# Optimization experiments

Measured on AMD Instinct MI355X. Metric: run time of the kernel, lower is better.

Reference implementation:

```python
import jax, jax.numpy as jnp
import numpy as np

ALPHA = 0.5        # self._alpha
MAX_COEFF = 10.0   # self._max_coeff
SHARPNESS = 5      # self._loss_sharpness

N_VARS = 1_000_000
N_CLAUSES = 4_000_000
N_EDGES = 12_000_000


def setup_inputs() -> dict:
    key = jax.random.key(0)
    k1, k2, k3, k4 = jax.random.split(key, 4)
    variable_prediction = jax.random.uniform(k1, (N_VARS, 1), dtype=jnp.float32)
    lits = jax.random.randint(k2, (N_EDGES,), 0, N_VARS, dtype=jnp.int32)
    clauses = jax.random.randint(k3, (N_EDGES,), 0, N_CLAUSES, dtype=jnp.int32)
    graph_map = jnp.stack([lits, clauses])  # [2, E]
    # literal polarity: +1 (positive literal) or -1 (negated literal)
    edge_feature = jnp.where(jax.random.bernoulli(k4, 0.5, (N_EDGES, 1)), 1.0, -1.0).astype(jnp.float32)
    return {
        "variable_prediction": variable_prediction,
        "graph_map": graph_map,
        "edge_feature": edge_feature,
        "num_clauses": N_CLAUSES,
        "global_step": jnp.array([100.0], dtype=jnp.float32),
        "eps": jnp.array([1e-10], dtype=jnp.float32),
    }


def reference(variable_prediction, graph_map, edge_feature, num_clauses, global_step, eps):
    # temperature coefficient: min(step^alpha, max_coeff)
    coeff = jnp.minimum(global_step ** ALPHA, MAX_COEFF)  # [1]
    lits = graph_map[0]     # [E] variable index per edge
    clauses = graph_map[1]  # [E] clause index per edge
    ef = edge_feature[:, 0]  # [E]

    # sparse mm (signed variable mask @ prediction) == signed gather
    edge_values = ef * variable_prediction[lits, 0]          # [E]
    edge_values = edge_values + (1.0 - ef) * 0.5             # negated literal -> 1 - p
    weights = jnp.exp(coeff * edge_values)                   # [E]

    # sparse mm (function mask @ .) == scatter-add over clauses
    nominator = jax.ops.segment_sum(weights * edge_values, clauses, num_segments=num_clauses)
    denominator = jax.ops.segment_sum(weights, clauses, num_segments=num_clauses)

    clause_value = denominator / jnp.maximum(nominator, eps)
    clause_value = 1.0 + (clause_value - 1.0) ** SHARPNESS
    return jnp.mean(jnp.log(jnp.maximum(clause_value, eps)))
```

## Files before the change

kernel.cpp:

```cpp
#include <hip/hip_runtime.h>
#include <math.h>


constexpr int   N_CLAUSES_C = 4000000;
constexpr int   BKT_SHIFT   = 12;
constexpr int   BKT_CLS     = 1 << BKT_SHIFT;
constexpr int   NB_TOTAL    = (N_CLAUSES_C + BKT_CLS - 1) >> BKT_SHIFT;
constexpr int   CAP         = 13056;
constexpr int   SC_THREADS  = 1024;
constexpr int   BATCH       = 8192;
constexpr int   NBATCH      = 3;
constexpr int   SC_CHUNK    = BATCH * NBATCH;
constexpr int   PR_THREADS  = 512;

typedef int v4i __attribute__((ext_vector_type(4)));

__device__ __forceinline__ uint32_t ev_enc(float ev) {
    return (__float_as_uint(ev) + 0x400u) >> 11;
}
__device__ __forceinline__ float ev_dec(uint32_t q) {
    return __uint_as_float(q << 11);
}

__device__ __forceinline__ void load_pair(const int* __restrict__ cls,
                                          const int* __restrict__ lits,
                                          int base, int c1, int (&cc)[8], int (&ll)[8]) {
    if (base + 8 <= c1) {
        v4i ca = __builtin_nontemporal_load((const v4i*)(cls  + base));
        v4i cb = __builtin_nontemporal_load((const v4i*)(cls  + base + 4));
        v4i la = __builtin_nontemporal_load((const v4i*)(lits + base));
        v4i lb = __builtin_nontemporal_load((const v4i*)(lits + base + 4));
        #pragma unroll
        for (int i = 0; i < 4; ++i) {
            cc[i] = ca[i]; cc[4 + i] = cb[i];
            ll[i] = la[i]; ll[4 + i] = lb[i];
        }
    } else {
        #pragma unroll
        for (int i = 0; i < 8; ++i) {
            int e = base + i;
            if (e < c1) { cc[i] = cls[e]; ll[i] = lits[e]; }
            else        { cc[i] = -1;     ll[i] = 0;       }
        }
    }
}

__device__ __forceinline__ void load_ef(const int* __restrict__ efi,
                                        int base, int c1, int (&ss)[8]) {
    if (base + 8 <= c1) {
        v4i fa = __builtin_nontemporal_load((const v4i*)(efi + base));
        v4i fb = __builtin_nontemporal_load((const v4i*)(efi + base + 4));
        #pragma unroll
        for (int i = 0; i < 4; ++i) { ss[i] = fa[i]; ss[4 + i] = fb[i]; }
    } else {
        #pragma unroll
        for (int i = 0; i < 8; ++i) { int e = base + i; ss[i] = (e < c1) ? efi[e] : 0; }
    }
}

__global__ __launch_bounds__(SC_THREADS, 8) void
scatter_kernel(const float* __restrict__ vp,
               const int* __restrict__ lits,
               const int* __restrict__ cls,
               const int* __restrict__ efi,
               uint32_t* __restrict__ payload,
               uint32_t* __restrict__ cursors,
               int n_edges, int b_lo, int b_hi) {
    __shared__ uint32_t bh[1024];
    __shared__ uint32_t bOff[1024];
    __shared__ uint32_t bb[NB_TOTAL];
    __shared__ uint32_t buf[BATCH];
    __shared__ uint16_t bufB[BATCH];
    __shared__ uint32_t totalS;

    const int tid  = threadIdx.x;
    const int lane = tid & 63;
    const int wv   = tid >> 6;
    const int nbp  = b_hi - b_lo;
    const int c0   = blockIdx.x * SC_CHUNK;
    const int c1   = min(n_edges, c0 + SC_CHUNK);
    const int nb   = (c1 - c0 + BATCH - 1) / BATCH;

    int cc[8], ll[8];
    load_pair(cls, lits, c0 + tid * 8, c1, cc, ll);
    bh[tid] = 0;
    __syncthreads();

    for (int k = 0; k < nb; ++k) {
        const int base = c0 + k * BATCH + tid * 8;

        int ss[8];
        load_ef(efi, base, c1, ss);
        float vv[8];
        #pragma unroll
        for (int i = 0; i < 8; ++i) vv[i] = (cc[i] >= 0) ? vp[ll[i]] : 0.0f;

        uint32_t meta[8];
        #pragma unroll
        for (int i = 0; i < 8; ++i) {
            meta[i] = 0xFFC00000u;
            if (cc[i] >= 0) {
                int b = cc[i] >> BKT_SHIFT;
                if (b >= b_lo && b < b_hi) {
                    uint32_t ib = (uint32_t)(b - b_lo);
                    uint32_t r  = atomicAdd(&bh[ib], 1u);
                    if (r < 1024u)
                        meta[i] = ((uint32_t)cc[i] & 4095u) | (r << 12) | (ib << 22);
                }
            }
        }
        __syncthreads();

        if (wv == 0) {
            const int jb = lane * 16;
            uint32_t t = 0;
            #pragma unroll
            for (int i = 0; i < 16; ++i) t += bh[jb + i];
            uint32_t x = t;
            #pragma unroll
            for (int d = 1; d < 64; d <<= 1) {
                uint32_t n = __shfl_up(x, (unsigned)d, 64);
                if (lane >= d) x += n;
            }
            uint32_t run = x - t;
            #pragma unroll
            for (int i = 0; i < 16; ++i) {
                uint32_t v = bh[jb + i];
                bOff[jb + i] = run;
                run += v;
            }
            if (lane == 63) totalS = x;
        } else {
            for (int i = tid - 64; i < nbp; i += SC_THREADS - 64) {
                uint32_t v = bh[i];
                bb[i] = v ? atomicAdd(&cursors[b_lo + i], v) : 0u;
            }
        }
        __syncthreads();

        #pragma unroll
        for (int i = 0; i < 8; ++i) {
            uint32_t ib = meta[i] >> 22;
            if (ib < 1023u) {
                float ev = (ss[i] >= 0) ? vv[i] : (1.0f - vv[i]);
                uint32_t s = bOff[ib] + ((meta[i] >> 12) & 1023u);
                buf[s]  = (ev_enc(ev) << BKT_SHIFT) | (meta[i] & 4095u);
                bufB[s] = (uint16_t)ib;
            }
        }
        bh[tid] = 0;
        if (k + 1 < nb)
            load_pair(cls, lits, c0 + (k + 1) * BATCH + tid * 8, c1, cc, ll);
        __syncthreads();

        const uint32_t tS = totalS;
        for (uint32_t s = tid; s < tS; s += SC_THREADS) {
            uint32_t ib   = bufB[s];
            uint32_t gpos = bb[ib] + (s - bOff[ib]);
            if (gpos < (uint32_t)CAP)
                payload[(size_t)ib * CAP + gpos] = buf[s];
        }
        __syncthreads();
    }
}

__global__ __launch_bounds__(PR_THREADS) void
process_kernel(const uint32_t* __restrict__ payload,
               const uint32_t* __restrict__ cursors,
               const float* __restrict__ gstep,
               const float* __restrict__ epsp,
               double* __restrict__ acc,
               int b_lo) {
    __shared__ uint32_t offp[BKT_CLS / 2];
    __shared__ uint32_t srt[CAP];
    __shared__ uint32_t wscan[8];
    __shared__ double   wsum[8];
    const int tid  = threadIdx.x;
    const int lane = tid & 63;
    const int wv   = tid >> 6;
    const int b    = b_lo + blockIdx.x;

    for (int j = tid; j < BKT_CLS / 2; j += PR_THREADS) offp[j] = 0;
    __syncthreads();

    const uint32_t cnt = min(cursors[b], (uint32_t)CAP);
    const uint32_t* pl = payload + (size_t)blockIdx.x * CAP;
    const uint32_t nv = cnt >> 2;

    for (uint32_t k = tid; k < nv; k += PR_THREADS) {
        uint4 p4 = ((const uint4*)pl)[k];
        uint32_t c;
        c = p4.x & (BKT_CLS - 1); atomicAdd(&offp[c >> 1], 1u << ((c & 1) << 4));
        c = p4.y & (BKT_CLS - 1); atomicAdd(&offp[c >> 1], 1u << ((c & 1) << 4));
        c = p4.z & (BKT_CLS - 1); atomicAdd(&offp[c >> 1], 1u << ((c & 1) << 4));
        c = p4.w & (BKT_CLS - 1); atomicAdd(&offp[c >> 1], 1u << ((c & 1) << 4));
    }
    for (uint32_t k = (nv << 2) + tid; k < cnt; k += PR_THREADS) {
        uint32_t c = pl[k] & (BKT_CLS - 1);
        atomicAdd(&offp[c >> 1], 1u << ((c & 1) << 4));
    }
    __syncthreads();

    uint32_t pk[4];
    const int jb = tid * 4;
    uint32_t t = 0;
    #pragma unroll
    for (int i = 0; i < 4; ++i) {
        pk[i] = offp[jb + i];
        t += (pk[i] & 0xFFFFu) + (pk[i] >> 16);
    }
    uint32_t x = t;
    #pragma unroll
    for (int d = 1; d < 64; d <<= 1) {
        uint32_t n = __shfl_up(x, (unsigned)d, 64);
        if (lane >= d) x += n;
    }
    if (lane == 63) wscan[wv] = x;
    __syncthreads();
    if (tid == 0) {
        uint32_t r = 0;
        #pragma unroll
        for (int w = 0; w < 8; ++w) { uint32_t tm = wscan[w]; wscan[w] = r; r += tm; }
    }
    __syncthreads();
    uint32_t run = (x - t) + wscan[wv];
    #pragma unroll
    for (int i = 0; i < 4; ++i) {
        uint32_t lo = pk[i] & 0xFFFFu, hi = pk[i] >> 16;
        offp[jb + i] = run | ((run + lo) << 16);
        run += lo + hi;
    }
    __syncthreads();

    for (uint32_t k = tid; k < nv; k += PR_THREADS) {
        uint4 p4 = ((const uint4*)pl)[k];
        #pragma unroll
        for (int j = 0; j < 4; ++j) {
            uint32_t p = (j == 0) ? p4.x : (j == 1) ? p4.y : (j == 2) ? p4.z : p4.w;
            uint32_t c = p & (BKT_CLS - 1);
            uint32_t sh = (c & 1) << 4;
            uint32_t r = atomicAdd(&offp[c >> 1], 1u << sh);
            srt[(r >> sh) & 0xFFFFu] = p;
        }
    }
    for (uint32_t k = (nv << 2) + tid; k < cnt; k += PR_THREADS) {
        uint32_t p = pl[k];
        uint32_t c = p & (BKT_CLS - 1);
        uint32_t sh = (c & 1) << 4;
        uint32_t r = atomicAdd(&offp[c >> 1], 1u << sh);
        srt[(r >> sh) & 0xFFFFu] = p;
    }
    __syncthreads();

    const float coeff = fminf(sqrtf(gstep[0]), 10.0f);
    const float eps   = epsp[0];
    const int gbase = b << BKT_SHIFT;
    double local = 0.0;
    for (int j = tid; j < BKT_CLS; j += PR_THREADS) {
        if (gbase + j < N_CLAUSES_C) {
            uint32_t e = (offp[j >> 1] >> ((j & 1) << 4)) & 0xFFFFu;
            uint32_t s = 0;
            if (j > 0) {
                int jm = j - 1;
                s = (offp[jm >> 1] >> ((jm & 1) << 4)) & 0xFFFFu;
            }
            float nom = 0.f, den = 0.f;
            for (uint32_t k = s; k < e; ++k) {
                float ev = ev_dec(srt[k] >> BKT_SHIFT);
                float w  = __expf(coeff * ev);
                nom = fmaf(w, ev, nom);
                den += w;
            }
            float cv = den / fmaxf(nom, eps);
            float tt = cv - 1.0f;
            float t2 = tt * tt;
            float cv2 = 1.0f + t2 * t2 * tt;
            local += (double)__logf(fmaxf(cv2, eps));
        }
    }
    #pragma unroll
    for (int off = 32; off > 0; off >>= 1) local += __shfl_down(local, off, 64);
    if (lane == 0) wsum[wv] = local;
    __syncthreads();
    if (tid == 0) {
        double s = 0.0;
        #pragma unroll
        for (int w = 0; w < 8; ++w) s += wsum[w];
        unsafeAtomicAdd(acc, s);
    }
}

__global__ void finalize_kernel(const double* __restrict__ acc,
                                const int* __restrict__ ncp,
                                float* __restrict__ out) {
    if (threadIdx.x == 0 && blockIdx.x == 0)
        out[0] = (float)(acc[0] / (double)ncp[0]);
}

extern "C" void kernel_launch(void* const* d_in, const int* in_sizes, int n_in,
                              void* d_out, int out_size, void* d_ws, size_t ws_size,
                              hipStream_t stream) {
    const float* vp    = (const float*)d_in[0];
    const int*   gmap  = (const int*)d_in[1];
    const float* ef    = (const float*)d_in[2];
    const int*   ncp   = (const int*)d_in[3];
    const float* gstep = (const float*)d_in[4];
    const float* epsp  = (const float*)d_in[5];
    float*       out   = (float*)d_out;

    const int n_edges = in_sizes[1] / 2;
    const int* lits = gmap;
    const int* cls  = gmap + n_edges;

    int P = 8;
    int nbp_max = (NB_TOTAL + 7) / 8;
    size_t cursors_off_w = (size_t)nbp_max * CAP;
    size_t acc_off_w = (cursors_off_w + NB_TOTAL + 1) & ~(size_t)1;
    const int cands[4] = {1, 2, 4, 8};
    for (int ci = 0; ci < 4; ++ci) {
        int cand = cands[ci];
        int nm = (NB_TOTAL + cand - 1) / cand;
        size_t pw = (size_t)nm * CAP;
        size_t cw = pw + NB_TOTAL;
        size_t aw = (cw + 1) & ~(size_t)1;
        size_t need = aw * 4 + 8;
        if (need <= ws_size) { P = cand; nbp_max = nm; cursors_off_w = pw; acc_off_w = aw; break; }
    }

    uint32_t* payload = (uint32_t*)d_ws;
    uint32_t* cursors = payload + cursors_off_w;
    double*   acc     = (double*)((uint32_t*)d_ws + acc_off_w);

    hipMemsetAsync(cursors, 0, (acc_off_w - cursors_off_w) * 4 + 8, stream);

    const int sc_blocks = (n_edges + SC_CHUNK - 1) / SC_CHUNK;
    for (int p = 0; p < P; ++p) {
        int b_lo = p * nbp_max;
        int b_hi = min(NB_TOTAL, b_lo + nbp_max);
        if (b_lo >= b_hi) continue;
        scatter_kernel<<<sc_blocks, SC_THREADS, 0, stream>>>(
            vp, lits, cls, (const int*)ef, payload, cursors, n_edges, b_lo, b_hi);
        process_kernel<<<b_hi - b_lo, PR_THREADS, 0, stream>>>(
            payload, cursors, gstep, epsp, acc, b_lo);
    }
    finalize_kernel<<<1, 64, 0, stream>>>(acc, ncp, out);
}
```

Before: 175.2 us.

## Double clause bucket width and split bucket processing across two half-blocks

Scatter buckets now cover 8192 clauses each instead of 4096, which halves the bucket count and the per-block histogram, offset and global cursor atomic work in the scatter kernel. The edge-value encoding gives up one more mantissa bit to make room for the wider clause index. The process kernel launches two blocks per bucket; each reads the whole bucket payload but only sorts and reduces the half of the clauses it owns, which keeps shared memory per block near its previous size. The cost is that every payload word is read twice, plus slightly coarser quantisation and new overflow clamps on the sort buffer.

```diff
diff --git a/kernel.cpp b/kernel.cpp
--- a/kernel.cpp
+++ b/kernel.cpp
@@ -3,10 +3,12 @@
 
 
 constexpr int   N_CLAUSES_C = 4000000;
-constexpr int   BKT_SHIFT   = 12;
+constexpr int   BKT_SHIFT   = 13;
 constexpr int   BKT_CLS     = 1 << BKT_SHIFT;
 constexpr int   NB_TOTAL    = (N_CLAUSES_C + BKT_CLS - 1) >> BKT_SHIFT;
-constexpr int   CAP         = 13056;
+constexpr int   CAP         = 25728;
+constexpr int   SUB_CLS     = 4096;
+constexpr int   SRT_CAP     = 13824;
 constexpr int   SC_THREADS  = 1024;
 constexpr int   BATCH       = 8192;
 constexpr int   NBATCH      = 3;
@@ -16,10 +18,10 @@
 typedef int v4i __attribute__((ext_vector_type(4)));
 
 __device__ __forceinline__ uint32_t ev_enc(float ev) {
-    return (__float_as_uint(ev) + 0x400u) >> 11;
+    return (__float_as_uint(ev) + 0x800u) >> 12;
 }
 __device__ __forceinline__ float ev_dec(uint32_t q) {
-    return __uint_as_float(q << 11);
+    return __uint_as_float(q << 12);
 }
 
 __device__ __forceinline__ void load_pair(const int* __restrict__ cls,
@@ -66,9 +68,9 @@
                uint32_t* __restrict__ payload,
                uint32_t* __restrict__ cursors,
                int n_edges, int b_lo, int b_hi) {
-    __shared__ uint32_t bh[1024];
-    __shared__ uint32_t bOff[1024];
-    __shared__ uint32_t bb[NB_TOTAL];
+    __shared__ uint32_t bh[512];
+    __shared__ uint32_t bOff[512];
+    __shared__ uint32_t bb[512];
     __shared__ uint32_t buf[BATCH];
     __shared__ uint16_t bufB[BATCH];
     __shared__ uint32_t totalS;
@@ -83,7 +85,7 @@
 
     int cc[8], ll[8];
     load_pair(cls, lits, c0 + tid * 8, c1, cc, ll);
-    bh[tid] = 0;
+    if (tid < 512) bh[tid] = 0;
     __syncthreads();
 
     for (int k = 0; k < nb; ++k) {
@@ -98,24 +100,24 @@
         uint32_t meta[8];
         #pragma unroll
         for (int i = 0; i < 8; ++i) {
-            meta[i] = 0xFFC00000u;
+            meta[i] = 0xFF800000u;
             if (cc[i] >= 0) {
                 int b = cc[i] >> BKT_SHIFT;
                 if (b >= b_lo && b < b_hi) {
                     uint32_t ib = (uint32_t)(b - b_lo);
                     uint32_t r  = atomicAdd(&bh[ib], 1u);
                     if (r < 1024u)
-                        meta[i] = ((uint32_t)cc[i] & 4095u) | (r << 12) | (ib << 22);
+                        meta[i] = ((uint32_t)cc[i] & 8191u) | (r << 13) | (ib << 23);
                 }
             }
         }
         __syncthreads();
 
         if (wv == 0) {
-            const int jb = lane * 16;
+            const int jb = lane * 8;
             uint32_t t = 0;
             #pragma unroll
-            for (int i = 0; i < 16; ++i) t += bh[jb + i];
+            for (int i = 0; i < 8; ++i) t += bh[jb + i];
             uint32_t x = t;
             #pragma unroll
             for (int d = 1; d < 64; d <<= 1) {
@@ -124,7 +126,7 @@
             }
             uint32_t run = x - t;
             #pragma unroll
-            for (int i = 0; i < 16; ++i) {
+            for (int i = 0; i < 8; ++i) {
                 uint32_t v = bh[jb + i];
                 bOff[jb + i] = run;
                 run += v;
@@ -140,15 +142,15 @@
 
         #pragma unroll
         for (int i = 0; i < 8; ++i) {
-            uint32_t ib = meta[i] >> 22;
-            if (ib < 1023u) {
+            uint32_t ib = meta[i] >> 23;
+            if (ib < 511u) {
                 float ev = (ss[i] >= 0) ? vv[i] : (1.0f - vv[i]);
-                uint32_t s = bOff[ib] + ((meta[i] >> 12) & 1023u);
-                buf[s]  = (ev_enc(ev) << BKT_SHIFT) | (meta[i] & 4095u);
+                uint32_t s = bOff[ib] + ((meta[i] >> 13) & 1023u);
+                buf[s]  = (ev_enc(ev) << BKT_SHIFT) | (meta[i] & 8191u);
                 bufB[s] = (uint16_t)ib;
             }
         }
-        bh[tid] = 0;
+        if (tid < 512) bh[tid] = 0;
         if (k + 1 < nb)
             load_pair(cls, lits, c0 + (k + 1) * BATCH + tid * 8, c1, cc, ll);
         __syncthreads();
@@ -170,34 +172,46 @@
                const float* __restrict__ gstep,
                const float* __restrict__ epsp,
                double* __restrict__ acc,
-               int b_lo) {
-    __shared__ uint32_t offp[BKT_CLS / 2];
-    __shared__ uint32_t srt[CAP];
+               int b_lo, int nbp) {
+    __shared__ uint32_t offp[SUB_CLS / 2];
+    __shared__ uint32_t srt[SRT_CAP];
     __shared__ uint32_t wscan[8];
     __shared__ double   wsum[8];
     const int tid  = threadIdx.x;
     const int lane = tid & 63;
     const int wv   = tid >> 6;
-    const int b    = b_lo + blockIdx.x;
-
-    for (int j = tid; j < BKT_CLS / 2; j += PR_THREADS) offp[j] = 0;
+
+    const int bid = blockIdx.x;
+    const int ibc = (bid >> 4) * 8 + (bid & 7);
+    const int half = (bid >> 3) & 1;
+    if (ibc >= nbp) return;
+    const int b = b_lo + ibc;
+    const uint32_t hmask = (uint32_t)half << 12;
+
+    for (int j = tid; j < SUB_CLS / 2; j += PR_THREADS) offp[j] = 0;
     __syncthreads();
 
     const uint32_t cnt = min(cursors[b], (uint32_t)CAP);
-    const uint32_t* pl = payload + (size_t)blockIdx.x * CAP;
+    const uint32_t* pl = payload + (size_t)ibc * CAP;
     const uint32_t nv = cnt >> 2;
 
     for (uint32_t k = tid; k < nv; k += PR_THREADS) {
         uint4 p4 = ((const uint4*)pl)[k];
-        uint32_t c;
-        c = p4.x & (BKT_CLS - 1); atomicAdd(&offp[c >> 1], 1u << ((c & 1) << 4));
-        c = p4.y & (BKT_CLS - 1); atomicAdd(&offp[c >> 1], 1u << ((c & 1) << 4));
-        c = p4.z & (BKT_CLS - 1); atomicAdd(&offp[c >> 1], 1u << ((c & 1) << 4));
-        c = p4.w & (BKT_CLS - 1); atomicAdd(&offp[c >> 1], 1u << ((c & 1) << 4));
+        #pragma unroll
+        for (int j = 0; j < 4; ++j) {
+            uint32_t p = (j == 0) ? p4.x : (j == 1) ? p4.y : (j == 2) ? p4.z : p4.w;
+            if ((p & 4096u) == hmask) {
+                uint32_t c = p & 4095u;
+                atomicAdd(&offp[c >> 1], 1u << ((c & 1) << 4));
+            }
+        }
     }
     for (uint32_t k = (nv << 2) + tid; k < cnt; k += PR_THREADS) {
-        uint32_t c = pl[k] & (BKT_CLS - 1);
-        atomicAdd(&offp[c >> 1], 1u << ((c & 1) << 4));
+        uint32_t p = pl[k];
+        if ((p & 4096u) == hmask) {
+            uint32_t c = p & 4095u;
+            atomicAdd(&offp[c >> 1], 1u << ((c & 1) << 4));
+        }
     }
     __syncthreads();
 
@@ -237,26 +251,32 @@
         #pragma unroll
         for (int j = 0; j < 4; ++j) {
             uint32_t p = (j == 0) ? p4.x : (j == 1) ? p4.y : (j == 2) ? p4.z : p4.w;
-            uint32_t c = p & (BKT_CLS - 1);
+            if ((p & 4096u) == hmask) {
+                uint32_t c = p & 4095u;
+                uint32_t sh = (c & 1) << 4;
+                uint32_t r = atomicAdd(&offp[c >> 1], 1u << sh);
+                uint32_t pos = (r >> sh) & 0xFFFFu;
+                if (pos < (uint32_t)SRT_CAP) srt[pos] = p;
+            }
+        }
+    }
+    for (uint32_t k = (nv << 2) + tid; k < cnt; k += PR_THREADS) {
+        uint32_t p = pl[k];
+        if ((p & 4096u) == hmask) {
+            uint32_t c = p & 4095u;
             uint32_t sh = (c & 1) << 4;
             uint32_t r = atomicAdd(&offp[c >> 1], 1u << sh);
-            srt[(r >> sh) & 0xFFFFu] = p;
-        }
-    }
-    for (uint32_t k = (nv << 2) + tid; k < cnt; k += PR_THREADS) {
-        uint32_t p = pl[k];
-        uint32_t c = p & (BKT_CLS - 1);
-        uint32_t sh = (c & 1) << 4;
-        uint32_t r = atomicAdd(&offp[c >> 1], 1u << sh);
-        srt[(r >> sh) & 0xFFFFu] = p;
+            uint32_t pos = (r >> sh) & 0xFFFFu;
+            if (pos < (uint32_t)SRT_CAP) srt[pos] = p;
+        }
     }
     __syncthreads();
 
     const float coeff = fminf(sqrtf(gstep[0]), 10.0f);
     const float eps   = epsp[0];
-    const int gbase = b << BKT_SHIFT;
+    const int gbase = (b << BKT_SHIFT) + (half << 12);
     double local = 0.0;
-    for (int j = tid; j < BKT_CLS; j += PR_THREADS) {
+    for (int j = tid; j < SUB_CLS; j += PR_THREADS) {
         if (gbase + j < N_CLAUSES_C) {
             uint32_t e = (offp[j >> 1] >> ((j & 1) << 4)) & 0xFFFFu;
             uint32_t s = 0;
@@ -264,6 +284,8 @@
                 int jm = j - 1;
                 s = (offp[jm >> 1] >> ((jm & 1) << 4)) & 0xFFFFu;
             }
+            e = min(e, (uint32_t)SRT_CAP);
+            s = min(s, e);
             float nom = 0.f, den = 0.f;
             for (uint32_t k = s; k < e; ++k) {
                 float ev = ev_dec(srt[k] >> BKT_SHIFT);
@@ -338,10 +360,12 @@
         int b_lo = p * nbp_max;
         int b_hi = min(NB_TOTAL, b_lo + nbp_max);
         if (b_lo >= b_hi) continue;
+        int nbp = b_hi - b_lo;
         scatter_kernel<<<sc_blocks, SC_THREADS, 0, stream>>>(
             vp, lits, cls, (const int*)ef, payload, cursors, n_edges, b_lo, b_hi);
-        process_kernel<<<b_hi - b_lo, PR_THREADS, 0, stream>>>(
-            payload, cursors, gstep, epsp, acc, b_lo);
+        int pr_grid = ((2 * nbp + 15) / 16) * 16;
+        process_kernel<<<pr_grid, PR_THREADS, 0, stream>>>(
+            payload, cursors, gstep, epsp, acc, b_lo, nbp);
     }
     finalize_kernel<<<1, 64, 0, stream>>>(acc, ncp, out);
 }
```

Measured after the change: 170.8 us. -2.5%, faster.

## Replace global-atomic bucket cursors with per-batch sorted segments and offset table

Applied to the files above, without the earlier changes.

The scatter kernel no longer reserves space in global per-bucket cursors with atomics. Each 8192-edge batch is counting-sorted by superbucket in shared memory and written out contiguously, and a uint16 offset table records where each bucket's segment starts. The process kernel then gathers its bucket's segments from every batch through that table. This removes the multi-pass partitioning, the global atomics and the cursor memset. In exchange, process blocks now run many short scalar loops over tiny per-batch segments, and uncoalesced reads from the strided table replace the vectorised contiguous loads.

```diff
diff --git a/kernel.cpp b/kernel.cpp
--- a/kernel.cpp
+++ b/kernel.cpp
@@ -3,10 +3,10 @@
 
 
 constexpr int   N_CLAUSES_C = 4000000;
-constexpr int   BKT_SHIFT   = 12;
-constexpr int   BKT_CLS     = 1 << BKT_SHIFT;
-constexpr int   NB_TOTAL    = (N_CLAUSES_C + BKT_CLS - 1) >> BKT_SHIFT;
-constexpr int   CAP         = 13056;
+constexpr int   SB_SHIFT    = 12;
+constexpr int   SB_CLS      = 1 << SB_SHIFT;
+constexpr int   NSB         = (N_CLAUSES_C + SB_CLS - 1) >> SB_SHIFT;
+constexpr int   SRT_CAP     = 13824;
 constexpr int   SC_THREADS  = 1024;
 constexpr int   BATCH       = 8192;
 constexpr int   NBATCH      = 3;
@@ -58,36 +58,34 @@
     }
 }
 
-__global__ __launch_bounds__(SC_THREADS, 8) void
+__global__ __launch_bounds__(SC_THREADS) void
 scatter_kernel(const float* __restrict__ vp,
                const int* __restrict__ lits,
                const int* __restrict__ cls,
                const int* __restrict__ efi,
                uint32_t* __restrict__ payload,
-               uint32_t* __restrict__ cursors,
-               int n_edges, int b_lo, int b_hi) {
+               uint16_t* __restrict__ tbl,
+               int n_edges, int npr) {
     __shared__ uint32_t bh[1024];
     __shared__ uint32_t bOff[1024];
-    __shared__ uint32_t bb[NB_TOTAL];
     __shared__ uint32_t buf[BATCH];
-    __shared__ uint16_t bufB[BATCH];
-    __shared__ uint32_t totalS;
 
     const int tid  = threadIdx.x;
     const int lane = tid & 63;
     const int wv   = tid >> 6;
-    const int nbp  = b_hi - b_lo;
     const int c0   = blockIdx.x * SC_CHUNK;
     const int c1   = min(n_edges, c0 + SC_CHUNK);
-    const int nb   = (c1 - c0 + BATCH - 1) / BATCH;
 
     int cc[8], ll[8];
+    uint32_t ent[8], pos[8];
+
     load_pair(cls, lits, c0 + tid * 8, c1, cc, ll);
     bh[tid] = 0;
     __syncthreads();
 
-    for (int k = 0; k < nb; ++k) {
+    for (int k = 0; k < NBATCH; ++k) {
         const int base = c0 + k * BATCH + tid * 8;
+        const int prod = blockIdx.x * NBATCH + k;
 
         int ss[8];
         load_ef(efi, base, c1, ss);
@@ -95,18 +93,31 @@
         #pragma unroll
         for (int i = 0; i < 8; ++i) vv[i] = (cc[i] >= 0) ? vp[ll[i]] : 0.0f;
 
-        uint32_t meta[8];
         #pragma unroll
         for (int i = 0; i < 8; ++i) {
-            meta[i] = 0xFFC00000u;
+            pos[i] = 0xFFFFFFFFu;
             if (cc[i] >= 0) {
-                int b = cc[i] >> BKT_SHIFT;
-                if (b >= b_lo && b < b_hi) {
-                    uint32_t ib = (uint32_t)(b - b_lo);
-                    uint32_t r  = atomicAdd(&bh[ib], 1u);
-                    if (r < 1024u)
-                        meta[i] = ((uint32_t)cc[i] & 4095u) | (r << 12) | (ib << 22);
-                }
+                uint32_t ib = (uint32_t)cc[i] >> SB_SHIFT;
+                uint32_t r  = atomicAdd(&bh[ib], 1u);
+                if (r < 2048u) pos[i] = (ib << 11) | r;
+            }
+        }
+
+        if (k > 0) {
+            const int basep = c0 + (k - 1) * BATCH;
+            if (basep < n_edges) {
+                uint4* dst = (uint4*)(payload + basep);
+                const uint4* src = (const uint4*)buf;
+                #pragma unroll
+                for (int i = 0; i < 2; ++i) dst[tid + i * SC_THREADS] = src[tid + i * SC_THREADS];
+            }
+        }
+
+        #pragma unroll
+        for (int i = 0; i < 8; ++i) {
+            if (pos[i] != 0xFFFFFFFFu) {
+                float ev = (ss[i] >= 0) ? vv[i] : (1.0f - vv[i]);
+                ent[i] = (ev_enc(ev) << SB_SHIFT) | ((uint32_t)cc[i] & (SB_CLS - 1));
             }
         }
         __syncthreads();
@@ -129,75 +140,60 @@
                 bOff[jb + i] = run;
                 run += v;
             }
-            if (lane == 63) totalS = x;
-        } else {
-            for (int i = tid - 64; i < nbp; i += SC_THREADS - 64) {
-                uint32_t v = bh[i];
-                bb[i] = v ? atomicAdd(&cursors[b_lo + i], v) : 0u;
-            }
-        }
-        __syncthreads();
-
-        #pragma unroll
-        for (int i = 0; i < 8; ++i) {
-            uint32_t ib = meta[i] >> 22;
-            if (ib < 1023u) {
-                float ev = (ss[i] >= 0) ? vv[i] : (1.0f - vv[i]);
-                uint32_t s = bOff[ib] + ((meta[i] >> 12) & 1023u);
-                buf[s]  = (ev_enc(ev) << BKT_SHIFT) | (meta[i] & 4095u);
-                bufB[s] = (uint16_t)ib;
-            }
-        }
-        bh[tid] = 0;
-        if (k + 1 < nb)
+        }
+        if (k + 1 < NBATCH)
             load_pair(cls, lits, c0 + (k + 1) * BATCH + tid * 8, c1, cc, ll);
         __syncthreads();
 
-        const uint32_t tS = totalS;
-        for (uint32_t s = tid; s < tS; s += SC_THREADS) {
-            uint32_t ib   = bufB[s];
-            uint32_t gpos = bb[ib] + (s - bOff[ib]);
-            if (gpos < (uint32_t)CAP)
-                payload[(size_t)ib * CAP + gpos] = buf[s];
-        }
+        #pragma unroll
+        for (int i = 0; i < 8; ++i) {
+            if (pos[i] != 0xFFFFFFFFu)
+                buf[bOff[pos[i] >> 11] + (pos[i] & 2047u)] = ent[i];
+        }
+        if (tid <= NSB)
+            tbl[(size_t)tid * npr + prod] = (uint16_t)bOff[tid];
+        bh[tid] = 0;
         __syncthreads();
+    }
+
+    const int basep = c0 + (NBATCH - 1) * BATCH;
+    if (basep < n_edges) {
+        uint4* dst = (uint4*)(payload + basep);
+        const uint4* src = (const uint4*)buf;
+        #pragma unroll
+        for (int i = 0; i < 2; ++i) dst[tid + i * SC_THREADS] = src[tid + i * SC_THREADS];
     }
 }
 
 __global__ __launch_bounds__(PR_THREADS) void
 process_kernel(const uint32_t* __restrict__ payload,
-               const uint32_t* __restrict__ cursors,
+               const uint16_t* __restrict__ tbl,
                const float* __restrict__ gstep,
                const float* __restrict__ epsp,
                double* __restrict__ acc,
-               int b_lo) {
-    __shared__ uint32_t offp[BKT_CLS / 2];
-    __shared__ uint32_t srt[CAP];
+               int npr) {
+    __shared__ uint32_t offp[SB_CLS / 2];
+    __shared__ uint32_t srt[SRT_CAP];
     __shared__ uint32_t wscan[8];
     __shared__ double   wsum[8];
     const int tid  = threadIdx.x;
     const int lane = tid & 63;
     const int wv   = tid >> 6;
-    const int b    = b_lo + blockIdx.x;
-
-    for (int j = tid; j < BKT_CLS / 2; j += PR_THREADS) offp[j] = 0;
-    __syncthreads();
-
-    const uint32_t cnt = min(cursors[b], (uint32_t)CAP);
-    const uint32_t* pl = payload + (size_t)blockIdx.x * CAP;
-    const uint32_t nv = cnt >> 2;
-
-    for (uint32_t k = tid; k < nv; k += PR_THREADS) {
-        uint4 p4 = ((const uint4*)pl)[k];
-        uint32_t c;
-        c = p4.x & (BKT_CLS - 1); atomicAdd(&offp[c >> 1], 1u << ((c & 1) << 4));
-        c = p4.y & (BKT_CLS - 1); atomicAdd(&offp[c >> 1], 1u << ((c & 1) << 4));
-        c = p4.z & (BKT_CLS - 1); atomicAdd(&offp[c >> 1], 1u << ((c & 1) << 4));
-        c = p4.w & (BKT_CLS - 1); atomicAdd(&offp[c >> 1], 1u << ((c & 1) << 4));
-    }
-    for (uint32_t k = (nv << 2) + tid; k < cnt; k += PR_THREADS) {
-        uint32_t c = pl[k] & (BKT_CLS - 1);
-        atomicAdd(&offp[c >> 1], 1u << ((c & 1) << 4));
+    const int j    = blockIdx.x;
+
+    for (int i = tid; i < SB_CLS / 2; i += PR_THREADS) offp[i] = 0;
+    __syncthreads();
+
+    const uint16_t* row0 = tbl + (size_t)j * npr;
+    const uint16_t* row1 = row0 + npr;
+
+    for (int pr = tid; pr < npr; pr += PR_THREADS) {
+        int o0 = row0[pr], o1 = row1[pr];
+        const uint32_t* seg = payload + (size_t)pr * BATCH + o0;
+        for (int i = 0; i < o1 - o0; ++i) {
+            uint32_t c = seg[i] & (SB_CLS - 1);
+            atomicAdd(&offp[c >> 1], 1u << ((c & 1) << 4));
+        }
     }
     __syncthreads();
 
@@ -232,41 +228,37 @@
     }
     __syncthreads();
 
-    for (uint32_t k = tid; k < nv; k += PR_THREADS) {
-        uint4 p4 = ((const uint4*)pl)[k];
-        #pragma unroll
-        for (int j = 0; j < 4; ++j) {
-            uint32_t p = (j == 0) ? p4.x : (j == 1) ? p4.y : (j == 2) ? p4.z : p4.w;
-            uint32_t c = p & (BKT_CLS - 1);
+    for (int pr = tid; pr < npr; pr += PR_THREADS) {
+        int o0 = row0[pr], o1 = row1[pr];
+        const uint32_t* seg = payload + (size_t)pr * BATCH + o0;
+        for (int i = 0; i < o1 - o0; ++i) {
+            uint32_t p = seg[i];
+            uint32_t c = p & (SB_CLS - 1);
             uint32_t sh = (c & 1) << 4;
             uint32_t r = atomicAdd(&offp[c >> 1], 1u << sh);
-            srt[(r >> sh) & 0xFFFFu] = p;
-        }
-    }
-    for (uint32_t k = (nv << 2) + tid; k < cnt; k += PR_THREADS) {
-        uint32_t p = pl[k];
-        uint32_t c = p & (BKT_CLS - 1);
-        uint32_t sh = (c & 1) << 4;
-        uint32_t r = atomicAdd(&offp[c >> 1], 1u << sh);
-        srt[(r >> sh) & 0xFFFFu] = p;
+            uint32_t ps = (r >> sh) & 0xFFFFu;
+            if (ps < (uint32_t)SRT_CAP) srt[ps] = p;
+        }
     }
     __syncthreads();
 
     const float coeff = fminf(sqrtf(gstep[0]), 10.0f);
     const float eps   = epsp[0];
-    const int gbase = b << BKT_SHIFT;
+    const int gbase = j << SB_SHIFT;
     double local = 0.0;
-    for (int j = tid; j < BKT_CLS; j += PR_THREADS) {
-        if (gbase + j < N_CLAUSES_C) {
-            uint32_t e = (offp[j >> 1] >> ((j & 1) << 4)) & 0xFFFFu;
+    for (int c = tid; c < SB_CLS; c += PR_THREADS) {
+        if (gbase + c < N_CLAUSES_C) {
+            uint32_t e = (offp[c >> 1] >> ((c & 1) << 4)) & 0xFFFFu;
             uint32_t s = 0;
-            if (j > 0) {
-                int jm = j - 1;
-                s = (offp[jm >> 1] >> ((jm & 1) << 4)) & 0xFFFFu;
-            }
+            if (c > 0) {
+                int cm = c - 1;
+                s = (offp[cm >> 1] >> ((cm & 1) << 4)) & 0xFFFFu;
+            }
+            e = min(e, (uint32_t)SRT_CAP);
+            s = min(s, e);
             float nom = 0.f, den = 0.f;
-            for (uint32_t k = s; k < e; ++k) {
-                float ev = ev_dec(srt[k] >> BKT_SHIFT);
+            for (uint32_t i = s; i < e; ++i) {
+                float ev = ev_dec(srt[i] >> SB_SHIFT);
                 float w  = __expf(coeff * ev);
                 nom = fmaf(w, ev, nom);
                 den += w;
@@ -312,36 +304,22 @@
     const int* lits = gmap;
     const int* cls  = gmap + n_edges;
 
-    int P = 8;
-    int nbp_max = (NB_TOTAL + 7) / 8;
-    size_t cursors_off_w = (size_t)nbp_max * CAP;
-    size_t acc_off_w = (cursors_off_w + NB_TOTAL + 1) & ~(size_t)1;
-    const int cands[4] = {1, 2, 4, 8};
-    for (int ci = 0; ci < 4; ++ci) {
-        int cand = cands[ci];
-        int nm = (NB_TOTAL + cand - 1) / cand;
-        size_t pw = (size_t)nm * CAP;
-        size_t cw = pw + NB_TOTAL;
-        size_t aw = (cw + 1) & ~(size_t)1;
-        size_t need = aw * 4 + 8;
-        if (need <= ws_size) { P = cand; nbp_max = nm; cursors_off_w = pw; acc_off_w = aw; break; }
-    }
+    const int sc_blocks = (n_edges + SC_CHUNK - 1) / SC_CHUNK;
+    const int npr       = sc_blocks * NBATCH;
+    const int nprod_a   = (n_edges + BATCH - 1) / BATCH;
 
     uint32_t* payload = (uint32_t*)d_ws;
-    uint32_t* cursors = payload + cursors_off_w;
-    double*   acc     = (double*)((uint32_t*)d_ws + acc_off_w);
-
-    hipMemsetAsync(cursors, 0, (acc_off_w - cursors_off_w) * 4 + 8, stream);
-
-    const int sc_blocks = (n_edges + SC_CHUNK - 1) / SC_CHUNK;
-    for (int p = 0; p < P; ++p) {
-        int b_lo = p * nbp_max;
-        int b_hi = min(NB_TOTAL, b_lo + nbp_max);
-        if (b_lo >= b_hi) continue;
-        scatter_kernel<<<sc_blocks, SC_THREADS, 0, stream>>>(
-            vp, lits, cls, (const int*)ef, payload, cursors, n_edges, b_lo, b_hi);
-        process_kernel<<<b_hi - b_lo, PR_THREADS, 0, stream>>>(
-            payload, cursors, gstep, epsp, acc, b_lo);
-    }
+    size_t pay_words  = (size_t)nprod_a * BATCH;
+    uint16_t* tbl     = (uint16_t*)(payload + pay_words);
+    size_t tbl_bytes  = (size_t)(NSB + 1) * npr * sizeof(uint16_t);
+    size_t acc_off    = (pay_words * 4 + tbl_bytes + 7) & ~(size_t)7;
+    double* acc       = (double*)((char*)d_ws + acc_off);
+
+    hipMemsetAsync(acc, 0, sizeof(double), stream);
+
+    scatter_kernel<<<sc_blocks, SC_THREADS, 0, stream>>>(
+        vp, lits, cls, (const int*)ef, payload, tbl, n_edges, npr);
+    process_kernel<<<NSB, PR_THREADS, 0, stream>>>(
+        payload, tbl, gstep, epsp, acc, npr);
     finalize_kernel<<<1, 64, 0, stream>>>(acc, ncp, out);
 }
```

After: 252.0 us. +43.8%, slower.
